# Kernel optimization log

Measured on AMD Instinct MI355X. Metric: run time of the kernel, lower is better.

The kernel has to match this reference:

```python
import jax, jax.numpy as jnp
import numpy as np

B, N, F_IN, F_OUT = 4, 4096, 64, 64
ALPHA = 0.2  # LeakyReLU negative slope
NEG_INF = -9e15


def setup_inputs() -> dict:
    key = jax.random.key(0)
    k1, k2, k3, k4 = jax.random.split(key, 4)
    h = jax.random.normal(k1, (B, N, F_IN), dtype=jnp.float32)
    adj = jax.random.randint(k2, (B, N, N), 0, 2, dtype=jnp.int32)
    # xavier_uniform-like init (gain 1.414)
    lim_w = 1.414 * np.sqrt(6.0 / (F_IN + F_OUT))
    W = jax.random.uniform(k3, (F_IN, F_OUT), dtype=jnp.float32, minval=-lim_w, maxval=lim_w)
    lim_a = 1.414 * np.sqrt(6.0 / (2 * F_OUT + 1))
    a = jax.random.uniform(k4, (2 * F_OUT, 1), dtype=jnp.float32, minval=-lim_a, maxval=lim_a)
    return {"h": h, "adj": adj, "W": W, "a": a}


def reference(h, adj, W, a):
    # Wh: [B, N, F_out]
    Wh = jnp.matmul(h, W)
    a1 = a[:F_OUT, 0]   # [F_out]
    a2 = a[F_OUT:, 0]   # [F_out]
    # e[b,i,j] = LeakyReLU(Wh[b,i].a1 + Wh[b,j].a2)  (decomposed, avoids O(N^2*2F) concat)
    ei = jnp.einsum('bnf,f->bn', Wh, a1)  # source term
    ej = jnp.einsum('bnf,f->bn', Wh, a2)  # target term
    e = ei[:, :, None] + ej[:, None, :]   # [B, N, N]
    e = jnp.where(e > 0, e, ALPHA * e)    # LeakyReLU
    att = jnp.where(adj > 0, e, NEG_INF)
    att = jax.nn.softmax(att, axis=-1)
    h_prime = jnp.matmul(att, Wh)         # [B, N, F_out]
    return jax.nn.elu(h_prime)
```

## Files before the change

### kernel.cpp

```cpp
#include <hip/hip_runtime.h>
#include <stdint.h>

#define N_NODES 4096
#define F_DIM   64
#define LRELU_ALPHA 0.2f

typedef _Float16 f16;
typedef __attribute__((ext_vector_type(8))) _Float16 half8;
typedef __attribute__((ext_vector_type(4))) float f32x4;

__global__ __launch_bounds__(256) void gat_pp(
    const float* __restrict__ h, const float* __restrict__ W,
    const float* __restrict__ a, const int* __restrict__ adj,
    float* __restrict__ ei, float* __restrict__ ej,
    f16* __restrict__ whB, float* __restrict__ blockmax,
    uint32_t* __restrict__ bits)
{
  __shared__ float sh_h[4][F_DIM];
  __shared__ f16 tile[F_DIM][16];
  __shared__ float wmax[4];
  const int t = threadIdx.x, w = t >> 6, lane = t & 63;
  const int bid = blockIdx.x;
  const int pid = bid / 5;

  if (bid % 5 != 0) {
    const int pk = bid - 1 - pid;
    const int row = pk * 4 + w;
    const int* rowp = adj + (size_t)row * N_NODES + lane;
    uint64_t* dst = (uint64_t*)(bits + (size_t)row * 128);

#pragma unroll 1
    for (int bch = 0; bch < 4; ++bch) {
      int v[16];
#pragma unroll
      for (int s = 0; s < 16; ++s)
        v[s] = rowp[(bch * 16 + s) * 64];
#pragma unroll
      for (int s = 0; s < 16; ++s) {
        const unsigned long long m = __ballot(v[s] > 0);
        if (lane == 0) dst[bch * 16 + s] = m;
      }
    }
    return;
  }

  const int n0 = pid * 16;
  const int b  = n0 >> 12;
  const int nl0 = n0 & (N_NODES - 1);

  float wcol[F_DIM];
#pragma unroll
  for (int k = 0; k < F_DIM; ++k) wcol[k] = W[k * F_DIM + lane];
  const float a1 = a[lane], a2 = a[F_DIM + lane];

  float runmax = -3e38f;
  for (int r = 0; r < 4; ++r) {
    const int loc = w * 4 + r;
    const int n = n0 + loc;
    const float hv = h[(size_t)n * F_DIM + lane];
    sh_h[w][lane] = hv;
    float wh = 0.f;
#pragma unroll
    for (int k = 0; k < F_DIM; k += 4) {
      const float4 hb = *(const float4*)(&sh_h[w][k]);
      wh = fmaf(hb.x, wcol[k + 0], wh);
      wh = fmaf(hb.y, wcol[k + 1], wh);
      wh = fmaf(hb.z, wcol[k + 2], wh);
      wh = fmaf(hb.w, wcol[k + 3], wh);
    }
    float s1 = wh * a1, s2 = wh * a2;
#pragma unroll
    for (int off = 32; off; off >>= 1) {
      s1 += __shfl_xor(s1, off);
      s2 += __shfl_xor(s2, off);
    }
    if (lane == 0) { ei[n] = s1; ej[n] = s2; }
    runmax = fmaxf(runmax, s2);
    tile[lane][loc] = (f16)wh;
  }
  if (lane == 0) wmax[w] = runmax;
  __syncthreads();

  {
    const int jc = nl0 >> 5;
    const int q0 = (nl0 >> 3) & 3;
    const int fc = t >> 6;
    const int r6 = t & 63;
    const int qp = r6 >> 5;
    const int m  = (r6 >> 1) & 15;
    const int xh = (t & 1) * 4;
    const int loc = qp * 8 + xh;
    f16* dst = whB + (((size_t)(b * 128 + jc)) * 4 + fc) * 512
                   + ((q0 + qp) * 16 + m) * 8 + xh;
    *(uint2*)dst = *(const uint2*)(&tile[fc * 16 + m][loc]);
  }
  if (t == 0)
    blockmax[pid] =
        fmaxf(fmaxf(wmax[0], wmax[1]), fmaxf(wmax[2], wmax[3]));
}

__global__ __launch_bounds__(512, 4) void gat_attn(
    const uint32_t* __restrict__ bits, const float* __restrict__ ei,
    const float* __restrict__ ej, const f16* __restrict__ whB,
    const float* __restrict__ blockmax, float* __restrict__ out)
{
  __shared__ float num_lds[8][32][F_DIM];
  __shared__ float den_lds[8][32];

  const int t = threadIdx.x, w = t >> 6, lane = t & 63;
  const int quad = lane >> 4, m = lane & 15;
  const int kq = quad * 8;
  const int b  = blockIdx.x >> 7;
  const int i0 = (blockIdx.x & 127) * 32;
  const int rowg0 = b * N_NODES + i0 + m;
  const int rowg1 = rowg0 + 16;

  float maxej;
  {
    const float4 v = *(const float4*)(blockmax + b * 256 + lane * 4);
    maxej = fmaxf(fmaxf(v.x, v.y), fmaxf(v.z, v.w));
#pragma unroll
    for (int off = 32; off; off >>= 1)
      maxej = fmaxf(maxej, __shfl_xor(maxej, off));
  }

  const float ei0 = ei[rowg0], ei1 = ei[rowg1];
  float bnd0 = ei0 + maxej;
  bnd0 = fmaxf(bnd0, LRELU_ALPHA * bnd0);
  float bnd1 = ei1 + maxej;
  bnd1 = fmaxf(bnd1, LRELU_ALPHA * bnd1);
  const float c10 = ei0 - bnd0, c20 = LRELU_ALPHA * ei0 - bnd0;
  const float c11 = ei1 - bnd1, c21 = LRELU_ALPHA * ei1 - bnd1;

  const float* ejb = ej + b * N_NODES + w * 512;
  const uint32_t* bitrow0 = bits + (size_t)rowg0 * 128 + w * 16;
  const uint32_t* bitrow1 = bits + (size_t)rowg1 * 128 + w * 16;
  const f16* whw = whB + ((size_t)(b * 128 + w * 16)) * 2048 + lane * 8;

  f32x4 acc0[4] = {{0.f,0.f,0.f,0.f},{0.f,0.f,0.f,0.f},
                   {0.f,0.f,0.f,0.f},{0.f,0.f,0.f,0.f}};
  f32x4 acc1[4] = {{0.f,0.f,0.f,0.f},{0.f,0.f,0.f,0.f},
                   {0.f,0.f,0.f,0.f},{0.f,0.f,0.f,0.f}};
  float dA0 = 0.f, dB0 = 0.f, dA1 = 0.f, dB1 = 0.f;

#pragma unroll 1
  for (int jc = 0; jc < 16; ++jc) {
    const uint32_t dw0 = bitrow0[jc];
    const uint32_t dw1 = bitrow1[jc];

    float ejA[8];
    *(float4*)(&ejA[0]) = *(const float4*)(ejb + jc * 32 + kq);
    *(float4*)(&ejA[4]) = *(const float4*)(ejb + jc * 32 + kq + 4);

    const f16* wjc = whw + (size_t)jc * 2048;
    half8 bf[4];
#pragma unroll
    for (int fc = 0; fc < 4; ++fc)
      bf[fc] = *(const half8*)(wjc + fc * 512);

    half8 pa0, pa1;
#pragma unroll
    for (int x = 0; x < 8; ++x) {
      const float e = ejA[x];
      const float g0 = fmaxf(e + c10, fmaf(LRELU_ALPHA, e, c20));
      const float g1 = fmaxf(e + c11, fmaf(LRELU_ALPHA, e, c21));
      const float p0 = ((dw0 >> (kq + x)) & 1u) ? __expf(g0) : 0.f;
      const float p1 = ((dw1 >> (kq + x)) & 1u) ? __expf(g1) : 0.f;
      pa0[x] = (f16)p0;
      pa1[x] = (f16)p1;
      if (x & 1) { dB0 += p0; dB1 += p1; }
      else       { dA0 += p0; dA1 += p1; }
    }

#pragma unroll
    for (int fc = 0; fc < 4; ++fc) {
      acc0[fc] = __builtin_amdgcn_mfma_f32_16x16x32_f16(pa0, bf[fc], acc0[fc], 0, 0, 0);
      acc1[fc] = __builtin_amdgcn_mfma_f32_16x16x32_f16(pa1, bf[fc], acc1[fc], 0, 0, 0);
    }
  }

  float den0 = dA0 + dB0, den1 = dA1 + dB1;
  den0 += __shfl_xor(den0, 16);
  den0 += __shfl_xor(den0, 32);
  den1 += __shfl_xor(den1, 16);
  den1 += __shfl_xor(den1, 32);
  if (lane < 16) {
    den_lds[w][lane] = den0;
    den_lds[w][lane + 16] = den1;
  }

#pragma unroll
  for (int fc = 0; fc < 4; ++fc)
#pragma unroll
    for (int rg = 0; rg < 4; ++rg) {
      num_lds[w][quad * 4 + rg][fc * 16 + m] = acc0[fc][rg];
      num_lds[w][16 + quad * 4 + rg][fc * 16 + m] = acc1[fc][rg];
    }
  __syncthreads();

#pragma unroll
  for (int k = 0; k < 4; ++k) {
    const int idx = k * 512 + t;
    const int il = idx >> 6, f = idx & 63;
    float num = 0.f, d = 0.f;
#pragma unroll
    for (int ww = 0; ww < 8; ++ww) {
      num += num_lds[ww][il][f];
      d   += den_lds[ww][il];
    }
    float v = (d > 0.f) ? (num / d) : 0.f;
    v = (v > 0.f) ? v : expm1f(v);
    out[((size_t)(b * N_NODES + i0 + il)) * F_DIM + f] = v;
  }
}

extern "C" void kernel_launch(void* const* d_in, const int* in_sizes, int n_in,
                              void* d_out, int out_size, void* d_ws, size_t ws_size,
                              hipStream_t stream) {
  const float* h   = (const float*)d_in[0];
  const int*   adj = (const int*)d_in[1];
  const float* W   = (const float*)d_in[2];
  const float* a   = (const float*)d_in[3];
  float* out = (float*)d_out;

  char* ws = (char*)d_ws;
  float*    ei       = (float*)ws;
  float*    ej       = (float*)(ws + 65536);
  float*    blockmax = (float*)(ws + 131072);
  f16*      whB      = (f16*)(ws + 135168);
  uint32_t* bits     = (uint32_t*)(ws + 2232320);

  hipLaunchKernelGGL(gat_pp, dim3(5120), dim3(256), 0, stream,
                     h, W, a, adj, ei, ej, whB, blockmax, bits);
  hipLaunchKernelGGL(gat_attn, dim3(512), dim3(512), 0, stream,
                     bits, ei, ej, whB, blockmax, out);
}
```

Before: 392.6 us.

## Fuse adjacency bit-packing into attention kernel via LDS bitmasks

Moves adjacency-to-bitmask packing out of the prep kernel and into the attention kernel. Each wave reads its own 32x512 slice of adj with int4 loads and ballots the results into LDS, reusing the num_lds buffer, before the MFMA loop. The bit layout is permuted to match the int4 lane mapping. This drops the global bits round-trip and a large part of the prep grid, but the 256 MB adj read now runs in only 512 attention blocks, which may hurt memory-level parallelism.

```diff
diff --git a/kernel.cpp b/kernel.cpp
--- a/kernel.cpp
+++ b/kernel.cpp
@@ -9,41 +9,17 @@
 typedef __attribute__((ext_vector_type(8))) _Float16 half8;
 typedef __attribute__((ext_vector_type(4))) float f32x4;
 
-__global__ __launch_bounds__(256) void gat_pp(
+__global__ __launch_bounds__(256) void gat_prep(
     const float* __restrict__ h, const float* __restrict__ W,
-    const float* __restrict__ a, const int* __restrict__ adj,
+    const float* __restrict__ a,
     float* __restrict__ ei, float* __restrict__ ej,
-    f16* __restrict__ whB, float* __restrict__ blockmax,
-    uint32_t* __restrict__ bits)
+    f16* __restrict__ whB, float* __restrict__ blockmax)
 {
   __shared__ float sh_h[4][F_DIM];
   __shared__ f16 tile[F_DIM][16];
   __shared__ float wmax[4];
   const int t = threadIdx.x, w = t >> 6, lane = t & 63;
-  const int bid = blockIdx.x;
-  const int pid = bid / 5;
-
-  if (bid % 5 != 0) {
-    const int pk = bid - 1 - pid;
-    const int row = pk * 4 + w;
-    const int* rowp = adj + (size_t)row * N_NODES + lane;
-    uint64_t* dst = (uint64_t*)(bits + (size_t)row * 128);
-
-#pragma unroll 1
-    for (int bch = 0; bch < 4; ++bch) {
-      int v[16];
-#pragma unroll
-      for (int s = 0; s < 16; ++s)
-        v[s] = rowp[(bch * 16 + s) * 64];
-#pragma unroll
-      for (int s = 0; s < 16; ++s) {
-        const unsigned long long m = __ballot(v[s] > 0);
-        if (lane == 0) dst[bch * 16 + s] = m;
-      }
-    }
-    return;
-  }
-
+  const int pid = blockIdx.x;
   const int n0 = pid * 16;
   const int b  = n0 >> 12;
   const int nl0 = n0 & (N_NODES - 1);
@@ -100,7 +76,7 @@
 }
 
 __global__ __launch_bounds__(512, 4) void gat_attn(
-    const uint32_t* __restrict__ bits, const float* __restrict__ ei,
+    const int* __restrict__ adj, const float* __restrict__ ei,
     const float* __restrict__ ej, const f16* __restrict__ whB,
     const float* __restrict__ blockmax, float* __restrict__ out)
 {
@@ -115,6 +91,33 @@
   const int rowg0 = b * N_NODES + i0 + m;
   const int rowg1 = rowg0 + 16;
 
+  uint64_t* mybits = (uint64_t*)(&num_lds[w][0][0]);
+
+  {
+    const int* base = adj + ((size_t)(b * N_NODES + i0)) * N_NODES + w * 512;
+#pragma unroll 1
+    for (int b8 = 0; b8 < 8; ++b8) {
+      int4 v[8];
+#pragma unroll
+      for (int s = 0; s < 8; ++s) {
+        const int r = b8 * 4 + (s >> 1), wi = s & 1;
+        v[s] = *((const int4*)(base + (size_t)r * N_NODES + wi * 256) + lane);
+      }
+#pragma unroll
+      for (int s = 0; s < 8; ++s) {
+        const int r = b8 * 4 + (s >> 1), wi = s & 1;
+        const uint64_t q0 = __ballot(v[s].x > 0);
+        const uint64_t q1 = __ballot(v[s].y > 0);
+        const uint64_t q2 = __ballot(v[s].z > 0);
+        const uint64_t q3 = __ballot(v[s].w > 0);
+        if (lane == 0) {
+          uint64_t* q = mybits + r * 8 + wi * 4;
+          q[0] = q0; q[1] = q1; q[2] = q2; q[3] = q3;
+        }
+      }
+    }
+  }
+
   float maxej;
   {
     const float4 v = *(const float4*)(blockmax + b * 256 + lane * 4);
@@ -133,8 +136,6 @@
   const float c11 = ei1 - bnd1, c21 = LRELU_ALPHA * ei1 - bnd1;
 
   const float* ejb = ej + b * N_NODES + w * 512;
-  const uint32_t* bitrow0 = bits + (size_t)rowg0 * 128 + w * 16;
-  const uint32_t* bitrow1 = bits + (size_t)rowg1 * 128 + w * 16;
   const f16* whw = whB + ((size_t)(b * 128 + w * 16)) * 2048 + lane * 8;
 
   f32x4 acc0[4] = {{0.f,0.f,0.f,0.f},{0.f,0.f,0.f,0.f},
@@ -144,40 +145,54 @@
   float dA0 = 0.f, dB0 = 0.f, dA1 = 0.f, dB1 = 0.f;
 
 #pragma unroll 1
-  for (int jc = 0; jc < 16; ++jc) {
-    const uint32_t dw0 = bitrow0[jc];
-    const uint32_t dw1 = bitrow1[jc];
-
-    float ejA[8];
-    *(float4*)(&ejA[0]) = *(const float4*)(ejb + jc * 32 + kq);
-    *(float4*)(&ejA[4]) = *(const float4*)(ejb + jc * 32 + kq + 4);
-
-    const f16* wjc = whw + (size_t)jc * 2048;
-    half8 bf[4];
-#pragma unroll
-    for (int fc = 0; fc < 4; ++fc)
-      bf[fc] = *(const half8*)(wjc + fc * 512);
-
-    half8 pa0, pa1;
-#pragma unroll
-    for (int x = 0; x < 8; ++x) {
-      const float e = ejA[x];
-      const float g0 = fmaxf(e + c10, fmaf(LRELU_ALPHA, e, c20));
-      const float g1 = fmaxf(e + c11, fmaf(LRELU_ALPHA, e, c21));
-      const float p0 = ((dw0 >> (kq + x)) & 1u) ? __expf(g0) : 0.f;
-      const float p1 = ((dw1 >> (kq + x)) & 1u) ? __expf(g1) : 0.f;
-      pa0[x] = (f16)p0;
-      pa1[x] = (f16)p1;
-      if (x & 1) { dB0 += p0; dB1 += p1; }
-      else       { dA0 += p0; dA1 += p1; }
-    }
-
-#pragma unroll
-    for (int fc = 0; fc < 4; ++fc) {
-      acc0[fc] = __builtin_amdgcn_mfma_f32_16x16x32_f16(pa0, bf[fc], acc0[fc], 0, 0, 0);
-      acc1[fc] = __builtin_amdgcn_mfma_f32_16x16x32_f16(pa1, bf[fc], acc1[fc], 0, 0, 0);
-    }
-  }
+  for (int wi = 0; wi < 2; ++wi) {
+    uint64_t q0[4], q1[4];
+#pragma unroll
+    for (int c = 0; c < 4; ++c) {
+      q0[c] = mybits[m * 8 + wi * 4 + c];
+      q1[c] = mybits[(m + 16) * 8 + wi * 4 + c];
+    }
+
+#pragma unroll 1
+    for (int j8 = 0; j8 < 8; ++j8) {
+      const int jc = wi * 8 + j8;
+      const int Lb = j8 * 8 + 2 * quad;
+
+      float ejA[8];
+      *(float4*)(&ejA[0]) = *(const float4*)(ejb + jc * 32 + kq);
+      *(float4*)(&ejA[4]) = *(const float4*)(ejb + jc * 32 + kq + 4);
+
+      const f16* wjc = whw + (size_t)jc * 2048;
+      half8 bf[4];
+#pragma unroll
+      for (int fc = 0; fc < 4; ++fc)
+        bf[fc] = *(const half8*)(wjc + fc * 512);
+
+      half8 pa0, pa1;
+#pragma unroll
+      for (int x = 0; x < 8; ++x) {
+        const float e = ejA[x];
+        const float g0 = fmaxf(e + c10, fmaf(LRELU_ALPHA, e, c20));
+        const float g1 = fmaxf(e + c11, fmaf(LRELU_ALPHA, e, c21));
+        const uint32_t bit0 = (uint32_t)(q0[x & 3] >> (Lb + (x >> 2))) & 1u;
+        const uint32_t bit1 = (uint32_t)(q1[x & 3] >> (Lb + (x >> 2))) & 1u;
+        const float p0 = bit0 ? __expf(g0) : 0.f;
+        const float p1 = bit1 ? __expf(g1) : 0.f;
+        pa0[x] = (f16)p0;
+        pa1[x] = (f16)p1;
+        if (x & 1) { dB0 += p0; dB1 += p1; }
+        else       { dA0 += p0; dA1 += p1; }
+      }
+
+#pragma unroll
+      for (int fc = 0; fc < 4; ++fc) {
+        acc0[fc] = __builtin_amdgcn_mfma_f32_16x16x32_f16(pa0, bf[fc], acc0[fc], 0, 0, 0);
+        acc1[fc] = __builtin_amdgcn_mfma_f32_16x16x32_f16(pa1, bf[fc], acc1[fc], 0, 0, 0);
+      }
+    }
+  }
+
+  __syncthreads();
 
   float den0 = dA0 + dB0, den1 = dA1 + dB1;
   den0 += __shfl_xor(den0, 16);
@@ -228,10 +243,9 @@
   float*    ej       = (float*)(ws + 65536);
   float*    blockmax = (float*)(ws + 131072);
   f16*      whB      = (f16*)(ws + 135168);
-  uint32_t* bits     = (uint32_t*)(ws + 2232320);
-
-  hipLaunchKernelGGL(gat_pp, dim3(5120), dim3(256), 0, stream,
-                     h, W, a, adj, ei, ej, whB, blockmax, bits);
+
+  hipLaunchKernelGGL(gat_prep, dim3(1024), dim3(256), 0, stream,
+                     h, W, a, ei, ej, whB, blockmax);
   hipLaunchKernelGGL(gat_attn, dim3(512), dim3(512), 0, stream,
-                     bits, ei, ej, whB, blockmax, out);
+                     adj, ei, ej, whB, blockmax, out);
 }
```

Measured after the change: 402.6 us. 2.6% more time.
